# Kernel optimization log

Measured on AMD Instinct MI355X. Metric: run time of the kernel, lower is better.

## Reference

```python
import jax, jax.numpy as jnp
import numpy as np

N = 100000
E = 3200000
IN_C, HID, EMB = 128, 128, 64


def setup_inputs() -> dict:
    key = jax.random.key(0)
    ks = jax.random.split(key, 8)
    x = jax.random.normal(ks[0], (N, IN_C), dtype=jnp.float32)
    edge_index = jax.random.randint(ks[1], (2, E), 0, N, dtype=jnp.int64)
    def lin(k, out_c, in_c):
        s = 1.0 / np.sqrt(in_c)
        return jax.random.uniform(k, (out_c, in_c), jnp.float32, -s, s)
    # PyG SAGEConv: lin_l (applied to aggregated neighbors, has bias), lin_r (root, no bias)
    return {
        "x": x,
        "edge_index": edge_index,
        "Wl1": lin(ks[2], HID, IN_C), "bl1": jnp.zeros((HID,), jnp.float32), "Wr1": lin(ks[3], HID, IN_C),
        "Wl2": lin(ks[4], HID, HID), "bl2": jnp.zeros((HID,), jnp.float32), "Wr2": lin(ks[5], HID, HID),
        "Wl3": lin(ks[6], EMB, HID), "bl3": jnp.zeros((EMB,), jnp.float32), "Wr3": lin(ks[7], EMB, HID),
    }


def _sage(x, src, dst, Wl, bl, Wr):
    # mean-aggregate neighbor features onto destination nodes
    msg = x[src]                                           # [E, C] gather
    agg = jax.ops.segment_sum(msg, dst, num_segments=N)    # [N, C]
    cnt = jax.ops.segment_sum(jnp.ones((src.shape[0],), x.dtype), dst, num_segments=N)
    mean = agg / jnp.maximum(cnt, 1.0)[:, None]
    return mean @ Wl.T + bl + x @ Wr.T


def reference(x, edge_index, Wl1, bl1, Wr1, Wl2, bl2, Wr2, Wl3, bl3, Wr3):
    src, dst = edge_index[0], edge_index[1]
    h = jax.nn.relu(_sage(x, src, dst, Wl1, bl1, Wr1))
    h = jax.nn.relu(_sage(h, src, dst, Wl2, bl2, Wr2))
    return _sage(h, src, dst, Wl3, bl3, Wr3)
```

## Files before the change

### kernel.cpp

```cpp
#include <hip/hip_runtime.h>


#define NN 100000
#define CHUNK 8192
#define NBKT 256
#define CAP 18432
#define PADCAP 7168
#define STRIDE (CAP + PADCAP)

typedef _Float16 half_t;
typedef __attribute__((ext_vector_type(4))) _Float16 half4v;
typedef __attribute__((ext_vector_type(8))) _Float16 half8v;
typedef __attribute__((ext_vector_type(4))) float float4v;

__global__ void init_misc(half_t* __restrict__ xh, half_t* __restrict__ hh,
                          int* __restrict__ cfill) {
    constexpr size_t SLAB32 = (size_t)(NN + 1) * 32;
    int t = threadIdx.x;
    cfill[t] = t * CAP;
    int sel = t >> 7;
    int cg = (t >> 5) & 3;
    int c = t & 31;
    half_t* p = sel ? hh : xh;
    p[(size_t)cg * SLAB32 + (size_t)NN * 32 + c] = (half_t)0.f;
}

__global__ __launch_bounds__(256) void partition_kernel(const int* __restrict__ src,
                                                        const int* __restrict__ dst,
                                                        int* __restrict__ cfill,
                                                        unsigned int* __restrict__ coarse,
                                                        int E) {
    __shared__ int h[NBKT];
    __shared__ int ssum[NBKT];
    __shared__ int off[NBKT];
    __shared__ unsigned int stage[CHUNK];
    int tid = threadIdx.x;
    h[tid] = 0;
    __syncthreads();
    int base = blockIdx.x * CHUNK;
    int nE = min(CHUNK, E - base);
    for (int i = tid; i < nE; i += 256) atomicAdd(&h[dst[base + i] >> 9], 1);
    __syncthreads();
    ssum[tid] = h[tid];
    __syncthreads();
    for (int o = 1; o < NBKT; o <<= 1) {
        int v = (tid >= o) ? ssum[tid - o] : 0;
        __syncthreads();
        ssum[tid] += v;
        __syncthreads();
    }
    off[tid] = ssum[tid] - h[tid];
    __syncthreads();
    for (int i = tid; i < nE; i += 256) {
        int d = dst[base + i];
        int s_ = src[base + i];
        int bin = d >> 9;
        int pos = atomicAdd(&off[bin], 1);
        stage[pos] = ((unsigned)(d & 511) << 17) | (unsigned)s_;
    }
    __syncthreads();
    int c = h[tid];
    int gs = 0;
    if (c) gs = atomicAdd(&cfill[tid], c);
    int lim = tid * CAP + CAP;
    int cc = min(c, max(0, lim - gs));
    int lstart = off[tid] - c;
    for (int k = 0; k < cc; k++) coarse[gs + k] = stage[lstart + k];
}

__global__ __launch_bounds__(256) void fine_sort_kernel(const unsigned int* __restrict__ coarse,
                                                        const int* __restrict__ cfill,
                                                        int* __restrict__ pbeg,
                                                        int* __restrict__ pend,
                                                        float* __restrict__ invdeg,
                                                        int* __restrict__ sorted_src, int n) {
    __shared__ int fh[1024];
    __shared__ int foff[1024];
    __shared__ int cur[1024];
    __shared__ int tsum[256];
    int b = blockIdx.x;
    int beg = b * CAP;
    int end = min(cfill[b], beg + CAP);
    int nb = end - beg;
    int tid = threadIdx.x;
#pragma unroll
    for (int j = 0; j < 4; j++) fh[tid * 4 + j] = 0;
    __syncthreads();
    for (int i = tid; i < nb; i += 256) {
        unsigned p = coarse[beg + i];
        int f = (int)((p >> 17) << 1) | ((p & 0x1FFFF) >= (NN / 2) ? 1 : 0);
        atomicAdd(&fh[f], 1);
    }
    __syncthreads();
    int b0 = tid * 4;
    int pcs[4];
    int s = 0;
#pragma unroll
    for (int j = 0; j < 4; j++) {
        int pc = (fh[b0 + j] + 7) & ~7;
        pcs[j] = pc;
        s += pc;
    }
    tsum[tid] = s;
    __syncthreads();
    for (int o = 1; o < 256; o <<= 1) {
        int v = (tid >= o) ? tsum[tid - o] : 0;
        __syncthreads();
        tsum[tid] += v;
        __syncthreads();
    }
    int run = (tid == 0) ? 0 : tsum[tid - 1];
    int pbase = b * STRIDE;
#pragma unroll
    for (int j = 0; j < 4; j++) {
        int ln = b0 + j;
        int rbeg = pbase + run;
        foff[ln] = run;
        cur[ln] = rbeg;
        int node = b * 512 + (ln >> 1);
        if (node < n) {
            pbeg[2 * node + (ln & 1)] = rbeg;
            pend[2 * node + (ln & 1)] = rbeg + pcs[j];
        }
        run += pcs[j];
    }
    __syncthreads();
    for (int i = tid; i < nb; i += 256) {
        unsigned p = coarse[beg + i];
        int f = (int)((p >> 17) << 1) | ((p & 0x1FFFF) >= (NN / 2) ? 1 : 0);
        int pos = atomicAdd(&cur[f], 1);
        sorted_src[pos] = (int)(p & 0x1FFFF);
    }
#pragma unroll
    for (int j = 0; j < 4; j++) {
        int ln = b0 + j;
        int raw = fh[ln];
        int rbeg = pbase + foff[ln];
        for (int k = raw; k < pcs[j]; k++) sorted_src[rbeg + k] = NN;
    }
    for (int ln = tid; ln < 512; ln += 256) {
        int nd = b * 512 + ln;
        if (nd < n) {
            int d = fh[2 * ln] + fh[2 * ln + 1];
            invdeg[nd] = d > 0 ? 1.0f / (float)d : 0.0f;
        }
    }
}

__global__ void cast_f2h(const float* __restrict__ in, half_t* __restrict__ out, int n4) {
    constexpr size_t SLAB32 = (size_t)(NN + 1) * 32;
    int t = blockIdx.x * blockDim.x + threadIdx.x;
    if (t < n4) {
        float4 v = *(const float4*)(in + (size_t)t * 4);
        half4v r = {(half_t)v.x, (half_t)v.y, (half_t)v.z, (half_t)v.w};
        int e = t * 4;
        int node = e >> 7;
        int c = e & 127;
        *(half4v*)(out + (size_t)(c >> 5) * SLAB32 + (size_t)node * 32 + (c & 31)) = r;
    }
}

template <int C_IN, int C_OUT>
__device__ inline void prep_one(const float* __restrict__ W, half_t* __restrict__ B, int t) {
    constexpr int NCT = C_OUT / 16;
    if (t >= C_IN * C_OUT) return;
    int jj = t & 7;
    int kq = (t >> 3) & 3;
    int c = (t >> 5) & 15;
    int ct = (t >> 9) % NCT;
    int chunk = t / (512 * NCT);
    int k = chunk * 32 + kq * 8 + jj;
    int j = ct * 16 + c;
    B[t] = (half_t)W[(size_t)j * C_IN + k];
}

__global__ __launch_bounds__(256) void prep_all(
    const float* __restrict__ Wl1, const float* __restrict__ Wr1,
    const float* __restrict__ Wl2, const float* __restrict__ Wr2,
    const float* __restrict__ Wl3, const float* __restrict__ Wr3,
    half_t* Bl1, half_t* Br1, half_t* Bl2, half_t* Br2, half_t* Bl3, half_t* Br3) {
    int b = blockIdx.x;
    int tid = threadIdx.x;
    if (b < 256) {
        int sel = b >> 6;
        int t = (b & 63) * 256 + tid;
        const float* W = sel == 0 ? Wl1 : sel == 1 ? Wr1 : sel == 2 ? Wl2 : Wr2;
        half_t* B = sel == 0 ? Bl1 : sel == 1 ? Br1 : sel == 2 ? Bl2 : Br2;
        prep_one<128, 128>(W, B, t);
    } else {
        int idx = b - 256;
        int sel = idx >> 5;
        int t = (idx & 31) * 256 + tid;
        prep_one<128, 64>(sel == 0 ? Wl3 : Wr3, sel == 0 ? Bl3 : Br3, t);
    }
}

__global__ __launch_bounds__(256) void gather_part128(
    const half_t* __restrict__ feat,
    const int* __restrict__ pbeg, const int* __restrict__ pend,
    const int* __restrict__ sorted_src, const float* __restrict__ invdeg,
    half_t* __restrict__ part0,
    half_t* __restrict__ part1,
    int n) {
    constexpr size_t SLAB32 = (size_t)(NN + 1) * 32;
    int slice = blockIdx.x & 7;
    int cg = slice >> 1;
    int s = slice & 1;
    int tid = threadIdx.x;
    int node = (blockIdx.x >> 3) * 32 + (tid >> 3);
    if (node >= n) return;
    int slot = (tid >> 2) & 1;
    int col = tid & 3;
    const char* bp = (const char*)feat + (size_t)cg * SLAB32 * 2 + (unsigned)(col << 4);
    int beg = pbeg[2 * node + s];
    int end = pend[2 * node + s];
    float a0 = 0.f, a1 = 0.f, a2 = 0.f, a3 = 0.f, a4 = 0.f, a5 = 0.f, a6 = 0.f, a7 = 0.f;
    int j = beg + slot;
    if (j < end) {
        int s0 = sorted_src[j];
        int s1 = sorted_src[j + 2];
        int s2 = sorted_src[j + 4];
        int s3 = sorted_src[j + 6];
        for (j += 8; j < end; j += 8) {
            int t0 = sorted_src[j];
            int t1 = sorted_src[j + 2];
            int t2 = sorted_src[j + 4];
            int t3 = sorted_src[j + 6];
            half8v v0 = *(const half8v*)(bp + ((unsigned)s0 << 6));
            half8v v1 = *(const half8v*)(bp + ((unsigned)s1 << 6));
            half8v v2 = *(const half8v*)(bp + ((unsigned)s2 << 6));
            half8v v3 = *(const half8v*)(bp + ((unsigned)s3 << 6));
            a0 += ((float)v0[0] + (float)v1[0]) + ((float)v2[0] + (float)v3[0]);
            a1 += ((float)v0[1] + (float)v1[1]) + ((float)v2[1] + (float)v3[1]);
            a2 += ((float)v0[2] + (float)v1[2]) + ((float)v2[2] + (float)v3[2]);
            a3 += ((float)v0[3] + (float)v1[3]) + ((float)v2[3] + (float)v3[3]);
            a4 += ((float)v0[4] + (float)v1[4]) + ((float)v2[4] + (float)v3[4]);
            a5 += ((float)v0[5] + (float)v1[5]) + ((float)v2[5] + (float)v3[5]);
            a6 += ((float)v0[6] + (float)v1[6]) + ((float)v2[6] + (float)v3[6]);
            a7 += ((float)v0[7] + (float)v1[7]) + ((float)v2[7] + (float)v3[7]);
            s0 = t0; s1 = t1; s2 = t2; s3 = t3;
        }
        half8v v0 = *(const half8v*)(bp + ((unsigned)s0 << 6));
        half8v v1 = *(const half8v*)(bp + ((unsigned)s1 << 6));
        half8v v2 = *(const half8v*)(bp + ((unsigned)s2 << 6));
        half8v v3 = *(const half8v*)(bp + ((unsigned)s3 << 6));
        a0 += ((float)v0[0] + (float)v1[0]) + ((float)v2[0] + (float)v3[0]);
        a1 += ((float)v0[1] + (float)v1[1]) + ((float)v2[1] + (float)v3[1]);
        a2 += ((float)v0[2] + (float)v1[2]) + ((float)v2[2] + (float)v3[2]);
        a3 += ((float)v0[3] + (float)v1[3]) + ((float)v2[3] + (float)v3[3]);
        a4 += ((float)v0[4] + (float)v1[4]) + ((float)v2[4] + (float)v3[4]);
        a5 += ((float)v0[5] + (float)v1[5]) + ((float)v2[5] + (float)v3[5]);
        a6 += ((float)v0[6] + (float)v1[6]) + ((float)v2[6] + (float)v3[6]);
        a7 += ((float)v0[7] + (float)v1[7]) + ((float)v2[7] + (float)v3[7]);
    }
    a0 += __shfl_xor(a0, 4); a1 += __shfl_xor(a1, 4);
    a2 += __shfl_xor(a2, 4); a3 += __shfl_xor(a3, 4);
    a4 += __shfl_xor(a4, 4); a5 += __shfl_xor(a5, 4);
    a6 += __shfl_xor(a6, 4); a7 += __shfl_xor(a7, 4);
    if (slot == 0) {
        float iv = invdeg[node];
        half8v r = {(half_t)(a0 * iv), (half_t)(a1 * iv), (half_t)(a2 * iv), (half_t)(a3 * iv),
                    (half_t)(a4 * iv), (half_t)(a5 * iv), (half_t)(a6 * iv), (half_t)(a7 * iv)};
        half_t* pp = (s == 0 ? part0 : part1);
        __builtin_nontemporal_store(r, (half8v*)(pp + (size_t)node * 128 + cg * 32 + col * 8));
    }
}

__global__ __launch_bounds__(256) void gather_part64(
    const half_t* __restrict__ z,
    const int* __restrict__ pbeg, const int* __restrict__ pend,
    const int* __restrict__ sorted_src, const float* __restrict__ invdeg,
    half_t* __restrict__ part0,
    half_t* __restrict__ part1,
    int n) {
    constexpr size_t SLAB32 = (size_t)(NN + 1) * 32;
    int slice = blockIdx.x & 3;
    int hg = slice >> 1;
    int s = slice & 1;
    int tid = threadIdx.x;
    int node = (blockIdx.x >> 2) * 32 + (tid >> 3);
    if (node >= n) return;
    int slot = (tid >> 2) & 1;
    int col = tid & 3;
    const char* bp = (const char*)z + (size_t)hg * SLAB32 * 2 + (unsigned)(col << 4);
    int beg = pbeg[2 * node + s];
    int end = pend[2 * node + s];
    float a0 = 0.f, a1 = 0.f, a2 = 0.f, a3 = 0.f, a4 = 0.f, a5 = 0.f, a6 = 0.f, a7 = 0.f;
    int j = beg + slot;
    if (j < end) {
        int s0 = sorted_src[j];
        int s1 = sorted_src[j + 2];
        int s2 = sorted_src[j + 4];
        int s3 = sorted_src[j + 6];
        for (j += 8; j < end; j += 8) {
            int t0 = sorted_src[j];
            int t1 = sorted_src[j + 2];
            int t2 = sorted_src[j + 4];
            int t3 = sorted_src[j + 6];
            half8v v0 = *(const half8v*)(bp + ((unsigned)s0 << 6));
            half8v v1 = *(const half8v*)(bp + ((unsigned)s1 << 6));
            half8v v2 = *(const half8v*)(bp + ((unsigned)s2 << 6));
            half8v v3 = *(const half8v*)(bp + ((unsigned)s3 << 6));
            a0 += ((float)v0[0] + (float)v1[0]) + ((float)v2[0] + (float)v3[0]);
            a1 += ((float)v0[1] + (float)v1[1]) + ((float)v2[1] + (float)v3[1]);
            a2 += ((float)v0[2] + (float)v1[2]) + ((float)v2[2] + (float)v3[2]);
            a3 += ((float)v0[3] + (float)v1[3]) + ((float)v2[3] + (float)v3[3]);
            a4 += ((float)v0[4] + (float)v1[4]) + ((float)v2[4] + (float)v3[4]);
            a5 += ((float)v0[5] + (float)v1[5]) + ((float)v2[5] + (float)v3[5]);
            a6 += ((float)v0[6] + (float)v1[6]) + ((float)v2[6] + (float)v3[6]);
            a7 += ((float)v0[7] + (float)v1[7]) + ((float)v2[7] + (float)v3[7]);
            s0 = t0; s1 = t1; s2 = t2; s3 = t3;
        }
        half8v v0 = *(const half8v*)(bp + ((unsigned)s0 << 6));
        half8v v1 = *(const half8v*)(bp + ((unsigned)s1 << 6));
        half8v v2 = *(const half8v*)(bp + ((unsigned)s2 << 6));
        half8v v3 = *(const half8v*)(bp + ((unsigned)s3 << 6));
        a0 += ((float)v0[0] + (float)v1[0]) + ((float)v2[0] + (float)v3[0]);
        a1 += ((float)v0[1] + (float)v1[1]) + ((float)v2[1] + (float)v3[1]);
        a2 += ((float)v0[2] + (float)v1[2]) + ((float)v2[2] + (float)v3[2]);
        a3 += ((float)v0[3] + (float)v1[3]) + ((float)v2[3] + (float)v3[3]);
        a4 += ((float)v0[4] + (float)v1[4]) + ((float)v2[4] + (float)v3[4]);
        a5 += ((float)v0[5] + (float)v1[5]) + ((float)v2[5] + (float)v3[5]);
        a6 += ((float)v0[6] + (float)v1[6]) + ((float)v2[6] + (float)v3[6]);
        a7 += ((float)v0[7] + (float)v1[7]) + ((float)v2[7] + (float)v3[7]);
    }
    a0 += __shfl_xor(a0, 4); a1 += __shfl_xor(a1, 4);
    a2 += __shfl_xor(a2, 4); a3 += __shfl_xor(a3, 4);
    a4 += __shfl_xor(a4, 4); a5 += __shfl_xor(a5, 4);
    a6 += __shfl_xor(a6, 4); a7 += __shfl_xor(a7, 4);
    if (slot == 0) {
        float iv = invdeg[node];
        half8v r = {(half_t)(a0 * iv), (half_t)(a1 * iv), (half_t)(a2 * iv), (half_t)(a3 * iv),
                    (half_t)(a4 * iv), (half_t)(a5 * iv), (half_t)(a6 * iv), (half_t)(a7 * iv)};
        half_t* pp = (s == 0 ? part0 : part1);
        __builtin_nontemporal_store(r, (half8v*)(pp + (size_t)node * 64 + hg * 32 + col * 8));
    }
}

__device__ inline half8v load_a32(const half_t* __restrict__ A, int rowc, int q, int ch) {
    constexpr size_t SLAB32 = (size_t)(NN + 1) * 32;
    return *(const half8v*)(A + (size_t)ch * SLAB32 + (size_t)rowc * 32 + q * 8);
}

template <bool FUSE_Z>
__global__ __launch_bounds__(256) void mfma_layer128(
    const half_t* __restrict__ rootSl,
    const half_t* __restrict__ part0, const half_t* __restrict__ part1,
    const half_t* __restrict__ Bl, const half_t* __restrict__ Br,
    const float* __restrict__ bias, half_t* __restrict__ outSl,
    const half_t* __restrict__ Bz, half_t* __restrict__ z_out, int n) {
    constexpr int NCT = 8;
    constexpr size_t SLAB32 = (size_t)(NN + 1) * 32;
    __shared__ __align__(16) half_t tile[4][16][136];
    int tid = threadIdx.x;
    int w = tid >> 6;
    int l = tid & 63;
    int c = l & 15;
    int q = l >> 4;
    int row = blockIdx.x * 64 + w * 16 + c;
    int rowc = min(row, n - 1);

    float4v acc[NCT];
#pragma unroll
    for (int i = 0; i < NCT; i++) acc[i] = (float4v){0.f, 0.f, 0.f, 0.f};

    {
        const half_t* B = Bl + (size_t)(c * 4 + q) * 8;
#pragma unroll
        for (int ch = 0; ch < 4; ch++) {
            half8v p0 = *(const half8v*)(part0 + (size_t)rowc * 128 + ch * 32 + q * 8);
            half8v p1 = *(const half8v*)(part1 + (size_t)rowc * 128 + ch * 32 + q * 8);
            half8v a = p0 + p1;
            half8v b[NCT];
#pragma unroll
            for (int t2 = 0; t2 < NCT; t2++)
                b[t2] = *(const half8v*)(B + (size_t)ch * (NCT * 512) + t2 * 512);
#pragma unroll
            for (int t2 = 0; t2 < NCT; t2++)
                acc[t2] = __builtin_amdgcn_mfma_f32_16x16x32_f16(a, b[t2], acc[t2], 0, 0, 0);
        }
    }
    {
        const half_t* B = Br + (size_t)(c * 4 + q) * 8;
#pragma unroll
        for (int ch = 0; ch < 4; ch++) {
            half8v a = load_a32(rootSl, rowc, q, ch);
            half8v b[NCT];
#pragma unroll
            for (int t2 = 0; t2 < NCT; t2++)
                b[t2] = *(const half8v*)(B + (size_t)ch * (NCT * 512) + t2 * 512);
#pragma unroll
            for (int t2 = 0; t2 < NCT; t2++)
                acc[t2] = __builtin_amdgcn_mfma_f32_16x16x32_f16(a, b[t2], acc[t2], 0, 0, 0);
        }
    }

    half_t (*T)[136] = tile[w];
    int lr0 = q * 4;
#pragma unroll
    for (int t2 = 0; t2 < NCT; t2++) {
        float bv = bias[t2 * 16 + c];
#pragma unroll
        for (int r = 0; r < 4; r++)
            T[lr0 + r][t2 * 16 + c] = (half_t)fmaxf(acc[t2][r] + bv, 0.f);
    }
    __syncthreads();

    int srow = l >> 2;
    int piece = l & 3;
    int grow = blockIdx.x * 64 + w * 16 + srow;
    if (grow < n) {
#pragma unroll
        for (int s = 0; s < 4; s++) {
            half8v v = *(const half8v*)(&T[srow][s * 32 + piece * 8]);
            *(half8v*)(outSl + (size_t)s * SLAB32 + (size_t)grow * 32 + piece * 8) = v;
        }
    }

    if (FUSE_Z) {
        float4v accz[4];
#pragma unroll
        for (int i = 0; i < 4; i++) accz[i] = (float4v){0.f, 0.f, 0.f, 0.f};
        const half_t* B = Bz + (size_t)(c * 4 + q) * 8;
#pragma unroll
        for (int ch = 0; ch < 4; ch++) {
            half8v a = *(const half8v*)(&T[c][ch * 32 + q * 8]);
            half8v b[4];
#pragma unroll
            for (int t2 = 0; t2 < 4; t2++)
                b[t2] = *(const half8v*)(B + (size_t)ch * (4 * 512) + t2 * 512);
#pragma unroll
            for (int t2 = 0; t2 < 4; t2++)
                accz[t2] = __builtin_amdgcn_mfma_f32_16x16x32_f16(a, b[t2], accz[t2], 0, 0, 0);
        }
#pragma unroll
        for (int t2 = 0; t2 < 4; t2++)
#pragma unroll
            for (int r = 0; r < 4; r++)
                T[lr0 + r][t2 * 16 + c] = (half_t)accz[t2][r];
        if (grow < n) {
#pragma unroll
            for (int s = 0; s < 2; s++) {
                half8v v = *(const half8v*)(&T[srow][s * 32 + piece * 8]);
                *(half8v*)(z_out + (size_t)s * SLAB32 + (size_t)grow * 32 + piece * 8) = v;
            }
        }
    }
}

__global__ __launch_bounds__(256) void mfma_final(
    const half_t* __restrict__ A_sl, const half_t* __restrict__ Bp,
    const half_t* __restrict__ pz0, const half_t* __restrict__ pz1,
    const float* __restrict__ bias, float* __restrict__ out, int n) {
    constexpr int NCT = 4;
    int tid = threadIdx.x;
    int w = tid >> 6;
    int l = tid & 63;
    int c = l & 15;
    int q = l >> 4;
    int row = blockIdx.x * 64 + w * 16 + c;
    int rowc = min(row, n - 1);

    float4v acc[NCT];
#pragma unroll
    for (int i = 0; i < NCT; i++) acc[i] = (float4v){0.f, 0.f, 0.f, 0.f};

    const half_t* B = Bp + (size_t)(c * 4 + q) * 8;
#pragma unroll
    for (int ch = 0; ch < 4; ch++) {
        half8v a = load_a32(A_sl, rowc, q, ch);
        half8v b[NCT];
#pragma unroll
        for (int t2 = 0; t2 < NCT; t2++)
            b[t2] = *(const half8v*)(B + (size_t)ch * (NCT * 512) + t2 * 512);
#pragma unroll
        for (int t2 = 0; t2 < NCT; t2++)
            acc[t2] = __builtin_amdgcn_mfma_f32_16x16x32_f16(a, b[t2], acc[t2], 0, 0, 0);
    }

    int orow0 = blockIdx.x * 64 + w * 16 + q * 4;
#pragma unroll
    for (int t2 = 0; t2 < NCT; t2++) {
        int col = t2 * 16 + c;
        float bv = bias[col];
#pragma unroll
        for (int r = 0; r < 4; r++) {
            int nrow = orow0 + r;
            if (nrow < n) {
                float m = (float)pz0[(size_t)nrow * 64 + col] +
                          (float)pz1[(size_t)nrow * 64 + col];
                out[(size_t)nrow * 64 + col] = acc[t2][r] + bv + m;
            }
        }
    }
}

extern "C" void kernel_launch(void* const* d_in, const int* in_sizes, int n_in,
                              void* d_out, int out_size, void* d_ws, size_t ws_size,
                              hipStream_t stream) {
    const float* x   = (const float*)d_in[0];
    const int*   ei  = (const int*)d_in[1];
    const float* Wl1 = (const float*)d_in[2];
    const float* bl1 = (const float*)d_in[3];
    const float* Wr1 = (const float*)d_in[4];
    const float* Wl2 = (const float*)d_in[5];
    const float* bl2 = (const float*)d_in[6];
    const float* Wr2 = (const float*)d_in[7];
    const float* Wl3 = (const float*)d_in[8];
    const float* bl3 = (const float*)d_in[9];
    const float* Wr3 = (const float*)d_in[10];

    const int N = NN;
    const int E = in_sizes[1] / 2;
    const int* src = ei;
    const int* dst = ei + E;

    const size_t SLABSZ = (size_t)(NN + 1) * 32;

    char* ws = (char*)d_ws;
    half_t* xh_sl = (half_t*)ws;
    half_t* hh_sl = xh_sl + 4 * SLABSZ;
    half_t* part0 = hh_sl + 4 * SLABSZ;
    half_t* part1 = part0 + (size_t)N * 128;
    half_t* z_grp  = xh_sl;
    half_t* partz0 = part0;
    half_t* partz1 = part1;
    int* cfill    = (int*)(part1 + (size_t)N * 128);
    int* pbeg     = cfill + 256;
    int* pend     = pbeg + 2 * N + 256;
    float* invdeg = (float*)(pend + 2 * N + 256);
    unsigned int* coarse = (unsigned int*)(invdeg + N);
    int* sorted_src = (int*)(coarse + (size_t)NBKT * CAP);
    half_t* Bl1 = (half_t*)(sorted_src + (size_t)NBKT * STRIDE + 64);
    half_t* Br1 = Bl1 + 128 * 128;
    half_t* Bl2 = Br1 + 128 * 128;
    half_t* Br2 = Bl2 + 128 * 128;
    half_t* Bl3 = Br2 + 128 * 128;
    half_t* Br3 = Bl3 + 64 * 128;

    cast_f2h<<<(N * 128 / 4 + 255) / 256, 256, 0, stream>>>(x, xh_sl, N * 128 / 4);
    prep_all<<<320, 256, 0, stream>>>(Wl1, Wr1, Wl2, Wr2, Wl3, Wr3,
                                      Bl1, Br1, Bl2, Br2, Bl3, Br3);
    init_misc<<<1, 256, 0, stream>>>(xh_sl, hh_sl, cfill);

    const int sort_blocks = (E + CHUNK - 1) / CHUNK;
    partition_kernel<<<sort_blocks, 256, 0, stream>>>(src, dst, cfill, coarse, E);
    fine_sort_kernel<<<(N + 511) / 512, 256, 0, stream>>>(coarse, cfill, pbeg, pend,
                                                          invdeg, sorted_src, N);

    const int g128_blocks = ((N + 31) / 32) * 8;
    const int g64_blocks  = ((N + 31) / 32) * 4;
    const int gemm_blocks = (N + 63) / 64;

    gather_part128<<<g128_blocks, 256, 0, stream>>>(xh_sl, pbeg, pend, sorted_src,
                                                    invdeg, part0, part1, N);
    mfma_layer128<false><<<gemm_blocks, 256, 0, stream>>>(
        xh_sl, part0, part1, Bl1, Br1, bl1, hh_sl, nullptr, nullptr, N);

    gather_part128<<<g128_blocks, 256, 0, stream>>>(hh_sl, pbeg, pend, sorted_src,
                                                    invdeg, part0, part1, N);
    mfma_layer128<true><<<gemm_blocks, 256, 0, stream>>>(
        hh_sl, part0, part1, Bl2, Br2, bl2, hh_sl, Bl3, z_grp, N);

    gather_part64<<<g64_blocks, 256, 0, stream>>>(z_grp, pbeg, pend, sorted_src,
                                                  invdeg, partz0, partz1, N);
    mfma_final<<<gemm_blocks, 256, 0, stream>>>(hh_sl, Br3, partz0, partz1,
                                                bl3, (float*)d_out, N);
}
```

Measured before the change: 536.0 us.

## Gather layer-1 neighbors from FP8 features, finer sort buckets, vectorized final epilogue

The input features are also quantized to FP8 during the cast, and the layer-1 mean aggregation now gathers 64-byte FP8 rows instead of FP16, halving the bytes fetched per edge in the first gather. The edge bucketing switches from 256 to 512 coarse buckets of 256 nodes each, with smaller per-bucket capacity and fine-sort blocks. The final GEMM epilogue stages results in shared memory so the partial-sum reads and output writes are done as vectorized row-contiguous accesses. FP8 quantization of x lowers the precision of the layer-1 aggregate, which risks tolerance failures.

```diff
diff --git a/kernel.cpp b/kernel.cpp
--- a/kernel.cpp
+++ b/kernel.cpp
@@ -3,26 +3,39 @@
 
 #define NN 100000
 #define CHUNK 8192
-#define NBKT 256
-#define CAP 18432
-#define PADCAP 7168
+#define NBKT 512
+#define NPOP 392
+#define CAP 9664
+#define PADCAP 3584
 #define STRIDE (CAP + PADCAP)
 
 typedef _Float16 half_t;
 typedef __attribute__((ext_vector_type(4))) _Float16 half4v;
 typedef __attribute__((ext_vector_type(8))) _Float16 half8v;
 typedef __attribute__((ext_vector_type(4))) float float4v;
-
-__global__ void init_misc(half_t* __restrict__ xh, half_t* __restrict__ hh,
-                          int* __restrict__ cfill) {
+typedef __attribute__((ext_vector_type(2))) float float2v;
+typedef __attribute__((ext_vector_type(4))) unsigned int uint4v;
+
+__global__ __launch_bounds__(512) void init_misc(half_t* __restrict__ xh,
+                                                 half_t* __restrict__ hh,
+                                                 unsigned char* __restrict__ xq,
+                                                 int* __restrict__ cfill) {
     constexpr size_t SLAB32 = (size_t)(NN + 1) * 32;
+    constexpr size_t SLAB64B = (size_t)(NN + 1) * 64;
     int t = threadIdx.x;
     cfill[t] = t * CAP;
-    int sel = t >> 7;
-    int cg = (t >> 5) & 3;
-    int c = t & 31;
-    half_t* p = sel ? hh : xh;
-    p[(size_t)cg * SLAB32 + (size_t)NN * 32 + c] = (half_t)0.f;
+    if (t < 256) {
+        int sel = t >> 7;
+        int cg = (t >> 5) & 3;
+        int c = t & 31;
+        half_t* p = sel ? hh : xh;
+        p[(size_t)cg * SLAB32 + (size_t)NN * 32 + c] = (half_t)0.f;
+    }
+    if (t < 32) {
+        int cg = t >> 4;
+        int i = t & 15;
+        ((unsigned int*)(xq + (size_t)cg * SLAB64B + (size_t)NN * 64))[i] = 0u;
+    }
 }
 
 __global__ __launch_bounds__(256) void partition_kernel(const int* __restrict__ src,
@@ -31,41 +44,50 @@
                                                         unsigned int* __restrict__ coarse,
                                                         int E) {
     __shared__ int h[NBKT];
-    __shared__ int ssum[NBKT];
     __shared__ int off[NBKT];
+    __shared__ int tsum[256];
     __shared__ unsigned int stage[CHUNK];
     int tid = threadIdx.x;
-    h[tid] = 0;
+    h[2 * tid] = 0;
+    h[2 * tid + 1] = 0;
     __syncthreads();
     int base = blockIdx.x * CHUNK;
     int nE = min(CHUNK, E - base);
-    for (int i = tid; i < nE; i += 256) atomicAdd(&h[dst[base + i] >> 9], 1);
-    __syncthreads();
-    ssum[tid] = h[tid];
-    __syncthreads();
-    for (int o = 1; o < NBKT; o <<= 1) {
-        int v = (tid >= o) ? ssum[tid - o] : 0;
+    for (int i = tid; i < nE; i += 256) atomicAdd(&h[dst[base + i] >> 8], 1);
+    __syncthreads();
+    int c0 = h[2 * tid], c1 = h[2 * tid + 1];
+    tsum[tid] = c0 + c1;
+    __syncthreads();
+    for (int o = 1; o < 256; o <<= 1) {
+        int v = (tid >= o) ? tsum[tid - o] : 0;
         __syncthreads();
-        ssum[tid] += v;
+        tsum[tid] += v;
         __syncthreads();
     }
-    off[tid] = ssum[tid] - h[tid];
+    int run = (tid == 0) ? 0 : tsum[tid - 1];
+    off[2 * tid] = run;
+    off[2 * tid + 1] = run + c0;
     __syncthreads();
     for (int i = tid; i < nE; i += 256) {
         int d = dst[base + i];
         int s_ = src[base + i];
-        int bin = d >> 9;
+        int bin = d >> 8;
         int pos = atomicAdd(&off[bin], 1);
-        stage[pos] = ((unsigned)(d & 511) << 17) | (unsigned)s_;
-    }
-    __syncthreads();
-    int c = h[tid];
-    int gs = 0;
-    if (c) gs = atomicAdd(&cfill[tid], c);
-    int lim = tid * CAP + CAP;
-    int cc = min(c, max(0, lim - gs));
-    int lstart = off[tid] - c;
-    for (int k = 0; k < cc; k++) coarse[gs + k] = stage[lstart + k];
+        stage[pos] = ((unsigned)(d & 255) << 17) | (unsigned)s_;
+    }
+    __syncthreads();
+#pragma unroll
+    for (int jj = 0; jj < 2; jj++) {
+        int bin = 2 * tid + jj;
+        int c = h[bin];
+        if (c) {
+            int gs = atomicAdd(&cfill[bin], c);
+            int lim = bin * CAP + CAP;
+            int cc = min(c, max(0, lim - gs));
+            int lstart = off[bin] - c;
+            for (int k = 0; k < cc; k++) coarse[gs + k] = stage[lstart + k];
+        }
+    }
 }
 
 __global__ __launch_bounds__(256) void fine_sort_kernel(const unsigned int* __restrict__ coarse,
@@ -74,17 +96,17 @@
                                                         int* __restrict__ pend,
                                                         float* __restrict__ invdeg,
                                                         int* __restrict__ sorted_src, int n) {
-    __shared__ int fh[1024];
-    __shared__ int foff[1024];
-    __shared__ int cur[1024];
+    __shared__ int fh[512];
+    __shared__ int foff[512];
+    __shared__ int cur[512];
     __shared__ int tsum[256];
     int b = blockIdx.x;
     int beg = b * CAP;
     int end = min(cfill[b], beg + CAP);
     int nb = end - beg;
     int tid = threadIdx.x;
-#pragma unroll
-    for (int j = 0; j < 4; j++) fh[tid * 4 + j] = 0;
+    fh[2 * tid] = 0;
+    fh[2 * tid + 1] = 0;
     __syncthreads();
     for (int i = tid; i < nb; i += 256) {
         unsigned p = coarse[beg + i];
@@ -92,11 +114,11 @@
         atomicAdd(&fh[f], 1);
     }
     __syncthreads();
-    int b0 = tid * 4;
-    int pcs[4];
+    int b0 = tid * 2;
+    int pcs[2];
     int s = 0;
 #pragma unroll
-    for (int j = 0; j < 4; j++) {
+    for (int j = 0; j < 2; j++) {
         int pc = (fh[b0 + j] + 7) & ~7;
         pcs[j] = pc;
         s += pc;
@@ -112,12 +134,12 @@
     int run = (tid == 0) ? 0 : tsum[tid - 1];
     int pbase = b * STRIDE;
 #pragma unroll
-    for (int j = 0; j < 4; j++) {
+    for (int j = 0; j < 2; j++) {
         int ln = b0 + j;
         int rbeg = pbase + run;
         foff[ln] = run;
         cur[ln] = rbeg;
-        int node = b * 512 + (ln >> 1);
+        int node = b * 256 + (ln >> 1);
         if (node < n) {
             pbeg[2 * node + (ln & 1)] = rbeg;
             pend[2 * node + (ln & 1)] = rbeg + pcs[j];
@@ -132,23 +154,23 @@
         sorted_src[pos] = (int)(p & 0x1FFFF);
     }
 #pragma unroll
-    for (int j = 0; j < 4; j++) {
+    for (int j = 0; j < 2; j++) {
         int ln = b0 + j;
         int raw = fh[ln];
         int rbeg = pbase + foff[ln];
         for (int k = raw; k < pcs[j]; k++) sorted_src[rbeg + k] = NN;
     }
-    for (int ln = tid; ln < 512; ln += 256) {
-        int nd = b * 512 + ln;
-        if (nd < n) {
-            int d = fh[2 * ln] + fh[2 * ln + 1];
-            invdeg[nd] = d > 0 ? 1.0f / (float)d : 0.0f;
-        }
-    }
-}
-
-__global__ void cast_f2h(const float* __restrict__ in, half_t* __restrict__ out, int n4) {
+    int nd = b * 256 + tid;
+    if (nd < n) {
+        int d = fh[2 * tid] + fh[2 * tid + 1];
+        invdeg[nd] = d > 0 ? 1.0f / (float)d : 0.0f;
+    }
+}
+
+__global__ void cast_f2h(const float* __restrict__ in, half_t* __restrict__ out,
+                         unsigned char* __restrict__ xq, int n4) {
     constexpr size_t SLAB32 = (size_t)(NN + 1) * 32;
+    constexpr size_t SLAB64B = (size_t)(NN + 1) * 64;
     int t = blockIdx.x * blockDim.x + threadIdx.x;
     if (t < n4) {
         float4 v = *(const float4*)(in + (size_t)t * 4);
@@ -157,6 +179,9 @@
         int node = e >> 7;
         int c = e & 127;
         *(half4v*)(out + (size_t)(c >> 5) * SLAB32 + (size_t)node * 32 + (c & 31)) = r;
+        unsigned int q = __builtin_amdgcn_cvt_pk_fp8_f32(v.x, v.y, 0, false);
+        q = __builtin_amdgcn_cvt_pk_fp8_f32(v.z, v.w, q, true);
+        *(unsigned int*)(xq + (size_t)(c >> 6) * SLAB64B + (size_t)node * 64 + (c & 63)) = q;
     }
 }
 
@@ -195,13 +220,85 @@
     }
 }
 
-__global__ __launch_bounds__(256) void gather_part128(
-    const half_t* __restrict__ feat,
+__device__ inline void acc16(float* a, uint4v w) {
+#pragma unroll
+    for (int j = 0; j < 4; j++) {
+        float2v lo = __builtin_amdgcn_cvt_pk_f32_fp8(w[j], false);
+        float2v hi = __builtin_amdgcn_cvt_pk_f32_fp8(w[j], true);
+        a[4 * j + 0] += lo.x;
+        a[4 * j + 1] += lo.y;
+        a[4 * j + 2] += hi.x;
+        a[4 * j + 3] += hi.y;
+    }
+}
+
+__global__ __launch_bounds__(256) void gather_q128(
+    const unsigned char* __restrict__ xq,
     const int* __restrict__ pbeg, const int* __restrict__ pend,
     const int* __restrict__ sorted_src, const float* __restrict__ invdeg,
     half_t* __restrict__ part0,
     half_t* __restrict__ part1,
     int n) {
+    constexpr size_t SLAB64B = (size_t)(NN + 1) * 64;
+    int slice = blockIdx.x & 3;
+    int cg = slice >> 1;
+    int s = slice & 1;
+    int tid = threadIdx.x;
+    int node = (blockIdx.x >> 2) * 32 + (tid >> 3);
+    if (node >= n) return;
+    int slot = (tid >> 2) & 1;
+    int col = tid & 3;
+    const char* bp = (const char*)xq + (size_t)cg * SLAB64B + (unsigned)(col << 4);
+    int beg = pbeg[2 * node + s];
+    int end = pend[2 * node + s];
+    float a[16];
+#pragma unroll
+    for (int i = 0; i < 16; i++) a[i] = 0.f;
+    int j = beg + slot;
+    if (j < end) {
+        int s0 = sorted_src[j];
+        int s1 = sorted_src[j + 2];
+        int s2 = sorted_src[j + 4];
+        int s3 = sorted_src[j + 6];
+        for (j += 8; j < end; j += 8) {
+            int t0 = sorted_src[j];
+            int t1 = sorted_src[j + 2];
+            int t2 = sorted_src[j + 4];
+            int t3 = sorted_src[j + 6];
+            uint4v w0 = *(const uint4v*)(bp + ((unsigned)s0 << 6));
+            uint4v w1 = *(const uint4v*)(bp + ((unsigned)s1 << 6));
+            uint4v w2 = *(const uint4v*)(bp + ((unsigned)s2 << 6));
+            uint4v w3 = *(const uint4v*)(bp + ((unsigned)s3 << 6));
+            acc16(a, w0); acc16(a, w1); acc16(a, w2); acc16(a, w3);
+            s0 = t0; s1 = t1; s2 = t2; s3 = t3;
+        }
+        uint4v w0 = *(const uint4v*)(bp + ((unsigned)s0 << 6));
+        uint4v w1 = *(const uint4v*)(bp + ((unsigned)s1 << 6));
+        uint4v w2 = *(const uint4v*)(bp + ((unsigned)s2 << 6));
+        uint4v w3 = *(const uint4v*)(bp + ((unsigned)s3 << 6));
+        acc16(a, w0); acc16(a, w1); acc16(a, w2); acc16(a, w3);
+    }
+#pragma unroll
+    for (int i = 0; i < 16; i++) a[i] += __shfl_xor(a[i], 4);
+    if (slot == 0) {
+        float iv = invdeg[node];
+        half8v r0, r1;
+#pragma unroll
+        for (int i = 0; i < 8; i++) {
+            r0[i] = (half_t)(a[i] * iv);
+            r1[i] = (half_t)(a[8 + i] * iv);
+        }
+        half_t* pp = (s == 0 ? part0 : part1) + (size_t)node * 128 + cg * 64 + col * 16;
+        __builtin_nontemporal_store(r0, (half8v*)pp);
+        __builtin_nontemporal_store(r1, (half8v*)(pp + 8));
+    }
+}
+
+__global__ __launch_bounds__(256) void gather_part128(
+    const half_t* __restrict__ feat,
+    const int* __restrict__ pbeg, const int* __restrict__ pend,
+    const int* __restrict__ sorted_src, const float* __restrict__ invdeg,
+    half_t* __restrict__ part0, half_t* __restrict__ part1, int n) {
     constexpr size_t SLAB32 = (size_t)(NN + 1) * 32;
     int slice = blockIdx.x & 7;
     int cg = slice >> 1;
@@ -270,9 +367,7 @@
     const half_t* __restrict__ z,
     const int* __restrict__ pbeg, const int* __restrict__ pend,
     const int* __restrict__ sorted_src, const float* __restrict__ invdeg,
-    half_t* __restrict__ part0,
-    half_t* __restrict__ part1,
-    int n) {
+    half_t* __restrict__ part0, half_t* __restrict__ part1, int n) {
     constexpr size_t SLAB32 = (size_t)(NN + 1) * 32;
     int slice = blockIdx.x & 3;
     int hg = slice >> 1;
@@ -453,6 +548,7 @@
     const half_t* __restrict__ pz0, const half_t* __restrict__ pz1,
     const float* __restrict__ bias, float* __restrict__ out, int n) {
     constexpr int NCT = 4;
+    __shared__ __align__(16) float Tf[4][16][68];
     int tid = threadIdx.x;
     int w = tid >> 6;
     int l = tid & 63;
@@ -478,19 +574,37 @@
             acc[t2] = __builtin_amdgcn_mfma_f32_16x16x32_f16(a, b[t2], acc[t2], 0, 0, 0);
     }
 
-    int orow0 = blockIdx.x * 64 + w * 16 + q * 4;
 #pragma unroll
     for (int t2 = 0; t2 < NCT; t2++) {
-        int col = t2 * 16 + c;
-        float bv = bias[col];
-#pragma unroll
-        for (int r = 0; r < 4; r++) {
-            int nrow = orow0 + r;
-            if (nrow < n) {
-                float m = (float)pz0[(size_t)nrow * 64 + col] +
-                          (float)pz1[(size_t)nrow * 64 + col];
-                out[(size_t)nrow * 64 + col] = acc[t2][r] + bv + m;
-            }
+        float bv = bias[t2 * 16 + c];
+#pragma unroll
+        for (int r = 0; r < 4; r++)
+            Tf[w][q * 4 + r][t2 * 16 + c] = acc[t2][r] + bv;
+    }
+    __syncthreads();
+
+    int row16 = l >> 2;
+    int piece = l & 3;
+    int grow = blockIdx.x * 64 + w * 16 + row16;
+    if (grow < n) {
+        const half_t* z0 = pz0 + (size_t)grow * 64 + piece * 16;
+        const half_t* z1 = pz1 + (size_t)grow * 64 + piece * 16;
+        half8v p0a = *(const half8v*)z0;
+        half8v p0b = *(const half8v*)(z0 + 8);
+        half8v p1a = *(const half8v*)z1;
+        half8v p1b = *(const half8v*)(z1 + 8);
+        float vals[16];
+#pragma unroll
+        for (int i = 0; i < 8; i++)
+            vals[i] = Tf[w][row16][piece * 16 + i] + (float)p0a[i] + (float)p1a[i];
+#pragma unroll
+        for (int i = 0; i < 8; i++)
+            vals[8 + i] = Tf[w][row16][piece * 16 + 8 + i] + (float)p0b[i] + (float)p1b[i];
+        float* op = out + (size_t)grow * 64 + piece * 16;
+#pragma unroll
+        for (int k = 0; k < 4; k++) {
+            float4 o = {vals[4 * k], vals[4 * k + 1], vals[4 * k + 2], vals[4 * k + 3]};
+            *(float4*)(op + k * 4) = o;
         }
     }
 }
@@ -516,6 +630,7 @@
     const int* dst = ei + E;
 
     const size_t SLABSZ = (size_t)(NN + 1) * 32;
+    const size_t SLAB64B = (size_t)(NN + 1) * 64;
 
     char* ws = (char*)d_ws;
     half_t* xh_sl = (half_t*)ws;
@@ -525,35 +640,37 @@
     half_t* z_grp  = xh_sl;
     half_t* partz0 = part0;
     half_t* partz1 = part1;
-    int* cfill    = (int*)(part1 + (size_t)N * 128);
-    int* pbeg     = cfill + 256;
+    unsigned char* xq = (unsigned char*)(part1 + (size_t)N * 128);
+    int* cfill    = (int*)(xq + 2 * SLAB64B);
+    int* pbeg     = cfill + 512;
     int* pend     = pbeg + 2 * N + 256;
     float* invdeg = (float*)(pend + 2 * N + 256);
     unsigned int* coarse = (unsigned int*)(invdeg + N);
-    int* sorted_src = (int*)(coarse + (size_t)NBKT * CAP);
-    half_t* Bl1 = (half_t*)(sorted_src + (size_t)NBKT * STRIDE + 64);
+    int* sorted_src = (int*)(coarse + (size_t)NPOP * CAP);
+    half_t* Bl1 = (half_t*)(sorted_src + (size_t)NPOP * STRIDE + 64);
     half_t* Br1 = Bl1 + 128 * 128;
     half_t* Bl2 = Br1 + 128 * 128;
     half_t* Br2 = Bl2 + 128 * 128;
     half_t* Bl3 = Br2 + 128 * 128;
     half_t* Br3 = Bl3 + 64 * 128;
 
-    cast_f2h<<<(N * 128 / 4 + 255) / 256, 256, 0, stream>>>(x, xh_sl, N * 128 / 4);
+    cast_f2h<<<(N * 128 / 4 + 255) / 256, 256, 0, stream>>>(x, xh_sl, xq, N * 128 / 4);
     prep_all<<<320, 256, 0, stream>>>(Wl1, Wr1, Wl2, Wr2, Wl3, Wr3,
                                       Bl1, Br1, Bl2, Br2, Bl3, Br3);
-    init_misc<<<1, 256, 0, stream>>>(xh_sl, hh_sl, cfill);
+    init_misc<<<1, 512, 0, stream>>>(xh_sl, hh_sl, xq, cfill);
 
     const int sort_blocks = (E + CHUNK - 1) / CHUNK;
     partition_kernel<<<sort_blocks, 256, 0, stream>>>(src, dst, cfill, coarse, E);
-    fine_sort_kernel<<<(N + 511) / 512, 256, 0, stream>>>(coarse, cfill, pbeg, pend,
+    fine_sort_kernel<<<(N + 255) / 256, 256, 0, stream>>>(coarse, cfill, pbeg, pend,
                                                           invdeg, sorted_src, N);
 
+    const int gq_blocks   = ((N + 31) / 32) * 4;
     const int g128_blocks = ((N + 31) / 32) * 8;
     const int g64_blocks  = ((N + 31) / 32) * 4;
     const int gemm_blocks = (N + 63) / 64;
 
-    gather_part128<<<g128_blocks, 256, 0, stream>>>(xh_sl, pbeg, pend, sorted_src,
-                                                    invdeg, part0, part1, N);
+    gather_q128<<<gq_blocks, 256, 0, stream>>>(xq, pbeg, pend, sorted_src,
+                                               invdeg, part0, part1, N);
     mfma_layer128<false><<<gemm_blocks, 256, 0, stream>>>(
         xh_sl, part0, part1, Bl1, Br1, bl1, hh_sl, nullptr, nullptr, N);
 
```

Result: faster. 493.1 us (-8.0%).
